# Kernel optimization log

Hardware: AMD Instinct MI355X
Metric: run time of the kernel (lower is better)

## Reference

```python
import jax, jax.numpy as jnp
import numpy as np

D, H, DK = 512, 8, 64
SCALE = 1.5 / 1.0  # gamma/tau, schedule='const'
NEG = -1e30


def _cross(x_q, x_kv, mask_kv, Wq, Wk, Wv, scale):
    # x_q: [B,Tq,D], x_kv: [B,Tk,D], mask_kv: [B,Tk] (1=keep, 0=mask)
    B, Tq, _ = x_q.shape
    Tk = x_kv.shape[1]
    q = (x_q @ Wq.T).reshape(B, Tq, H, DK).transpose(0, 2, 1, 3)
    k = (x_kv @ Wk.T).reshape(B, Tk, H, DK).transpose(0, 2, 1, 3)
    v = (x_kv @ Wv.T).reshape(B, Tk, H, DK).transpose(0, 2, 1, 3)
    logits = jnp.einsum('bhqd,bhkd->bhqk', q, k) * (scale / jnp.sqrt(jnp.float32(DK)))
    if mask_kv is not None:
        logits = jnp.where(mask_kv[:, None, None, :] == 0, NEG, logits)
    attn = jax.nn.softmax(logits, axis=-1)
    out = jnp.einsum('bhqk,bhkd->bhqd', attn, v)
    return out.transpose(0, 2, 1, 3).reshape(B, Tq, D)


def setup_inputs() -> dict:
    key = jax.random.key(0)
    ks = jax.random.split(key, 12)
    B, T = 4, 2048
    inp = {
        'skel_seq': jax.random.normal(ks[0], (B, T, D), jnp.float32),
        'sens_seq': jax.random.normal(ks[1], (B, T, D), jnp.float32),
        'mask_skel': jax.random.randint(ks[2], (B, T), 0, 2, jnp.int32),
        'mask_sens': jax.random.randint(ks[3], (B, T), 0, 2, jnp.int32),
    }
    s = 1.0 / np.sqrt(D)
    names = ['Wq_s2e', 'Wk_e', 'Wv_e', 'Wq_e2s', 'Wk_s', 'Wv_s', 'Wo_s', 'Wo_e']
    for i, n in enumerate(names):
        inp[n] = jax.random.normal(ks[4 + i], (D, D), jnp.float32) * s
    return inp


def reference(skel_seq, sens_seq, mask_skel, mask_sens,
              Wq_s2e, Wk_e, Wv_e, Wq_e2s, Wk_s, Wv_s, Wo_s, Wo_e):
    # skel queries attend over sensor keys/values
    s2e = _cross(skel_seq, sens_seq, mask_sens, Wq_s2e, Wk_e, Wv_e, SCALE) @ Wo_e.T
    # sensor queries attend over skeleton keys/values
    e2s = _cross(sens_seq, skel_seq, mask_skel, Wq_e2s, Wk_s, Wv_s, SCALE) @ Wo_s.T
    return (e2s, s2e)
```

## Files before the change

kernel.cpp:

```cpp
#include <hip/hip_runtime.h>
#include <hip/hip_bf16.h>

#define T_SEQ 2048
#define N_TOK 4194304
#define W_ELEM 262144


typedef float f32x4  __attribute__((ext_vector_type(4)));
typedef short bf16x8 __attribute__((ext_vector_type(8)));

#define SCALE_Q 0.27050532f

__device__ __forceinline__ unsigned short f2b(float f) {
    __hip_bfloat16 h = __float2bfloat16(f);
    return *reinterpret_cast<unsigned short*>(&h);
}

__device__ __forceinline__ int pack2bf(float lo, float hi) {
    return ((int)f2b(hi) << 16) | (int)f2b(lo);
}

__device__ __forceinline__ bf16x8 ldg8(const unsigned short* p) {
    union { int4 i; bf16x8 b; } u;
    u.i = *reinterpret_cast<const int4*>(p);
    return u.b;
}

__device__ __forceinline__ float fexp2(float x) {
#if __has_builtin(__builtin_amdgcn_exp2f)
    return __builtin_amdgcn_exp2f(x);
#else
    return exp2f(x);
#endif
}

typedef unsigned int u32_g __attribute__((address_space(1)));
typedef unsigned int u32_l __attribute__((address_space(3)));
__device__ __forceinline__ void gload_lds16(const void* g, void* l) {
    __builtin_amdgcn_global_load_lds((const u32_g*)g, (u32_l*)l, 16, 0, 0);
}

__global__ __launch_bounds__(256)
void prep_bias(const int* __restrict__ ms, const int* __restrict__ mk,
               float* __restrict__ dst)
{
    const int i = (blockIdx.x * 256 + threadIdx.x) * 8;
    const int* m = (i >> 13) ? mk : ms;
    const int rem = i & 8191;
    const int4 a = *reinterpret_cast<const int4*>(&m[rem]);
    const int4 b = *reinterpret_cast<const int4*>(&m[rem + 4]);
    float4 f0, f1;
    f0.x = a.x ? 0.0f : -3e38f; f0.y = a.y ? 0.0f : -3e38f;
    f0.z = a.z ? 0.0f : -3e38f; f0.w = a.w ? 0.0f : -3e38f;
    f1.x = b.x ? 0.0f : -3e38f; f1.y = b.y ? 0.0f : -3e38f;
    f1.z = b.z ? 0.0f : -3e38f; f1.w = b.w ? 0.0f : -3e38f;
    *reinterpret_cast<float4*>(&dst[i])     = f0;
    *reinterpret_cast<float4*>(&dst[i + 4]) = f1;
}

__global__ __launch_bounds__(256)
void to_bf16(const float* __restrict__ s0, const float* __restrict__ s1,
             const float* __restrict__ w0, const float* __restrict__ w1,
             const float* __restrict__ w2, const float* __restrict__ w3,
             const float* __restrict__ w4, const float* __restrict__ w5,
             unsigned short* __restrict__ dst)
{
    const int y = blockIdx.y;
    const float* src;
    size_t off; int n;
    switch (y) {
        case 0: src = s0; off = 0;                          n = N_TOK;  break;
        case 1: src = s1; off = N_TOK;                      n = N_TOK;  break;
        case 2: src = w0; off = 2 * (size_t)N_TOK;              n = W_ELEM; break;
        case 3: src = w1; off = 2 * (size_t)N_TOK + 1 * W_ELEM; n = W_ELEM; break;
        case 4: src = w2; off = 2 * (size_t)N_TOK + 2 * W_ELEM; n = W_ELEM; break;
        case 5: src = w3; off = 2 * (size_t)N_TOK + 3 * W_ELEM; n = W_ELEM; break;
        case 6: src = w4; off = 2 * (size_t)N_TOK + 4 * W_ELEM; n = W_ELEM; break;
        default: src = w5; off = 2 * (size_t)N_TOK + 5 * W_ELEM; n = W_ELEM; break;
    }
    const int idx = (blockIdx.x * 256 + threadIdx.x) * 8;
    if (idx >= n) return;
    const float4 a = *reinterpret_cast<const float4*>(src + idx);
    const float4 b = *reinterpret_cast<const float4*>(src + idx + 4);
    int4 o;
    o.x = pack2bf(a.x, a.y); o.y = pack2bf(a.z, a.w);
    o.z = pack2bf(b.x, b.y); o.w = pack2bf(b.z, b.w);
    *reinterpret_cast<int4*>(dst + off + idx) = o;
}

#define MF_SETUP                                                               \
    __shared__ short Asm[64][72];                                              \
    __shared__ short Wsm[64][72];                                              \
    const int tid  = threadIdx.x;                                              \
    const int lane = tid & 63;                                                 \
    const int w4   = tid >> 6;                                                 \
    const int nl   = lane & 15;                                                \
    const int quad = lane >> 4;                                                \
    const int n0 = blockIdx.x * 64;                                            \
    const int m0 = blockIdx.y * 64;                                            \
    const int arow = tid >> 2;                                                 \
    const int acol = (tid & 3) * 16;                                           \
    f32x4 acc[4] = {};

#define MF_WRITE_W                                                             \
    {                                                                          \
        int4 x;                                                                \
        x.x = pack2bf(wv[0].x, wv[0].y); x.y = pack2bf(wv[0].z, wv[0].w);      \
        x.z = pack2bf(wv[1].x, wv[1].y); x.w = pack2bf(wv[1].z, wv[1].w);      \
        *reinterpret_cast<int4*>(&Wsm[arow][acol]) = x;                        \
        x.x = pack2bf(wv[2].x, wv[2].y); x.y = pack2bf(wv[2].z, wv[2].w);      \
        x.z = pack2bf(wv[3].x, wv[3].y); x.w = pack2bf(wv[3].z, wv[3].w);      \
        *reinterpret_cast<int4*>(&Wsm[arow][acol + 8]) = x;                    \
    }

#define MF_MMA_LOOP                                                            \
    _Pragma("unroll")                                                          \
    for (int kc = 0; kc < 2; ++kc) {                                           \
        const bf16x8 a = *reinterpret_cast<const bf16x8*>(                     \
            &Asm[w4 * 16 + nl][kc * 32 + quad * 8]);                           \
        _Pragma("unroll")                                                      \
        for (int c = 0; c < 4; ++c) {                                          \
            const bf16x8 bf = *reinterpret_cast<const bf16x8*>(                \
                &Wsm[c * 16 + nl][kc * 32 + quad * 8]);                        \
            acc[c] = __builtin_amdgcn_mfma_f32_16x16x32_bf16(a, bf, acc[c],    \
                                                             0, 0, 0);         \
        }                                                                      \
    }

#define MF_CWRITE_PROJ                                                         \
    if (!trans) {                                                              \
        _Pragma("unroll")                                                      \
        for (int c = 0; c < 4; ++c)                                            \
            _Pragma("unroll")                                                  \
            for (int r = 0; r < 4; ++r)                                        \
                C[(size_t)(m0 + w4 * 16 + quad * 4 + r) * 512 + n0 + c * 16 + nl] = \
                    f2b(acc[c][r] * alpha);                                    \
    } else {                                                                   \
        const int b  = m0 >> 11;                                               \
        const int t0 = (m0 & 2047) + w4 * 16 + quad * 4;                       \
        _Pragma("unroll")                                                      \
        for (int c = 0; c < 4; ++c) {                                          \
            const int n = n0 + c * 16 + nl;                                    \
            ushort4 o;                                                         \
            o.x = f2b(acc[c][0]);                                              \
            o.y = f2b(acc[c][1]);                                              \
            o.z = f2b(acc[c][2]);                                              \
            o.w = f2b(acc[c][3]);                                              \
            *reinterpret_cast<ushort4*>(C + (size_t)(b * 512 + n) * T_SEQ + t0) = o; \
        }                                                                      \
    }

__global__ __launch_bounds__(256)
void proj_all(const float* __restrict__ skel, const float* __restrict__ sens,
              const float* __restrict__ Wq1, const float* __restrict__ Wk1,
              const float* __restrict__ Wv1, const float* __restrict__ Wq2,
              const float* __restrict__ Wk2, const float* __restrict__ Wv2,
              unsigned short* __restrict__ Q1, unsigned short* __restrict__ K1,
              unsigned short* __restrict__ Vt1, unsigned short* __restrict__ Q2,
              unsigned short* __restrict__ K2, unsigned short* __restrict__ Vt2,
              int zbase)
{
    const int z = zbase + blockIdx.z;
    const float* A; const float* W; unsigned short* C;
    float alpha = 1.0f; bool trans = false;
    switch (z) {
        case 0:  A = skel; W = Wq1; C = Q1; alpha = SCALE_Q; break;
        case 1:  A = sens; W = Wk1; C = K1; break;
        case 2:  A = sens; W = Wv1; C = Vt1; trans = true; break;
        case 3:  A = sens; W = Wq2; C = Q2; alpha = SCALE_Q; break;
        case 4:  A = skel; W = Wk2; C = K2; break;
        default: A = skel; W = Wv2; C = Vt2; trans = true; break;
    }

    MF_SETUP
    const float* ap = A + (size_t)(m0 + arow) * 512 + acol;
    const float* wp = W + (size_t)(n0 + arow) * 512 + acol;
    float4 av[4], wv[4];
    #pragma unroll
    for (int j = 0; j < 4; ++j) {
        av[j] = *reinterpret_cast<const float4*>(ap + 4 * j);
        wv[j] = *reinterpret_cast<const float4*>(wp + 4 * j);
    }
    for (int it = 0; it < 8; ++it) {
        __syncthreads();
        {
            int4 x;
            x.x = pack2bf(av[0].x, av[0].y); x.y = pack2bf(av[0].z, av[0].w);
            x.z = pack2bf(av[1].x, av[1].y); x.w = pack2bf(av[1].z, av[1].w);
            *reinterpret_cast<int4*>(&Asm[arow][acol]) = x;
            x.x = pack2bf(av[2].x, av[2].y); x.y = pack2bf(av[2].z, av[2].w);
            x.z = pack2bf(av[3].x, av[3].y); x.w = pack2bf(av[3].z, av[3].w);
            *reinterpret_cast<int4*>(&Asm[arow][acol + 8]) = x;
        }
        MF_WRITE_W
        __syncthreads();
        if (it < 7) {
            const float* apn = ap + (it + 1) * 64;
            const float* wpn = wp + (it + 1) * 64;
            #pragma unroll
            for (int j = 0; j < 4; ++j) {
                av[j] = *reinterpret_cast<const float4*>(apn + 4 * j);
                wv[j] = *reinterpret_cast<const float4*>(wpn + 4 * j);
            }
        }
        MF_MMA_LOOP
    }
    MF_CWRITE_PROJ
}

__global__ __launch_bounds__(256, 2)
void proj_fused(const unsigned short* __restrict__ skb,
                const unsigned short* __restrict__ snb,
                const unsigned short* __restrict__ wball,
                unsigned short* __restrict__ Q1, unsigned short* __restrict__ K1,
                unsigned short* __restrict__ Vt1, unsigned short* __restrict__ Q2,
                unsigned short* __restrict__ K2, unsigned short* __restrict__ Vt2)
{
    __shared__ short Al[2][64][64];
    __shared__ short Wl[2][256][64];

    const int o  = blockIdx.x;
    const int wg = (o & 7) * 192 + (o >> 3);
    const int z  = wg >> 8;
    const int mt = (wg >> 1) & 127;
    const int xh = wg & 1;

    const unsigned short* A = (z == 0 || z >= 4) ? skb : snb;
    const unsigned short* W = wball + (size_t)z * W_ELEM;
    unsigned short* C;
    switch (z) {
        case 0: C = Q1;  break;
        case 1: C = K1;  break;
        case 2: C = Vt1; break;
        case 3: C = Q2;  break;
        case 4: C = K2;  break;
        default: C = Vt2; break;
    }
    const bool trans = (z == 2 || z == 5);
    const float alpha = (z == 0 || z == 3) ? SCALE_Q : 1.0f;

    const int tid  = threadIdx.x;
    const int w    = tid >> 6;
    const int lane = tid & 63;
    const int nl   = lane & 15;
    const int quad = lane >> 4;
    const int r8   = lane >> 3;
    const int cg   = (lane & 7) ^ r8;

    const int m0g = mt * 64;
    const int n0  = xh * 256;

    const unsigned short* Ab = A + (size_t)m0g * 512 + cg * 8;
    const unsigned short* Wb = W + (size_t)n0  * 512 + cg * 8;

    f32x4 acc[16] = {};

    auto stage = [&](int it, int buf) {
        const int k0 = it * 64;
        #pragma unroll
        for (int g = 0; g < 2; ++g) {
            const int rr = w * 16 + g * 8;
            gload_lds16(Ab + (size_t)(rr + r8) * 512 + k0, &Al[buf][rr][0]);
        }
        #pragma unroll
        for (int g = 0; g < 8; ++g) {
            const int rr = w * 64 + g * 8;
            gload_lds16(Wb + (size_t)(rr + r8) * 512 + k0, &Wl[buf][rr][0]);
        }
    };

    stage(0, 0);
    asm volatile("s_waitcnt vmcnt(0)" ::: "memory");
    __syncthreads();

    const int sw = nl & 7;
    for (int it = 0; it < 8; ++it) {
        const int buf = it & 1;
        if (it < 7) stage(it + 1, buf ^ 1);
        #pragma unroll
        for (int kc = 0; kc < 2; ++kc) {
            const bf16x8 a = *reinterpret_cast<const bf16x8*>(
                &Al[buf][w * 16 + nl][((kc * 4 + quad) ^ sw) * 8]);
            #pragma unroll
            for (int c = 0; c < 16; ++c) {
                const bf16x8 b = *reinterpret_cast<const bf16x8*>(
                    &Wl[buf][c * 16 + nl][((kc * 4 + quad) ^ sw) * 8]);
                acc[c] = __builtin_amdgcn_mfma_f32_16x16x32_bf16(a, b, acc[c],
                                                                 0, 0, 0);
            }
        }
        asm volatile("s_waitcnt vmcnt(0)" ::: "memory");
        __syncthreads();
    }

    short* ep = &Wl[0][0][0];
    if (!trans) {
        short (*Cl)[264] = reinterpret_cast<short (*)[264]>(ep);
        #pragma unroll
        for (int c = 0; c < 16; ++c)
            #pragma unroll
            for (int r = 0; r < 4; ++r)
                Cl[w * 16 + quad * 4 + r][c * 16 + nl] =
                    (short)f2b(acc[c][r] * alpha);
        __syncthreads();
        const int lr = tid >> 2;
        const int sb = (tid & 3) * 64;
        unsigned short* cp = C + (size_t)(m0g + lr) * 512 + n0 + sb;
        #pragma unroll
        for (int j = 0; j < 8; ++j)
            *reinterpret_cast<int4*>(cp + j * 8) =
                *reinterpret_cast<const int4*>(&Cl[lr][sb + j * 8]);
    } else {
        short (*Tl)[72] = reinterpret_cast<short (*)[72]>(ep);
        #pragma unroll
        for (int c = 0; c < 16; ++c) {
            int* dst = reinterpret_cast<int*>(&Tl[c * 16 + nl][w * 16 + quad * 4]);
            dst[0] = pack2bf(acc[c][0], acc[c][1]);
            dst[1] = pack2bf(acc[c][2], acc[c][3]);
        }
        __syncthreads();
        const int bq = m0g >> 11;
        const int t0 = m0g & 2047;
        #pragma unroll
        for (int g = 0; g < 4; ++g) {
            const int nr = g * 64 + (tid >> 2);
            const int tc = (tid & 3) * 16;
            unsigned short* vp = C + (size_t)(bq * 512 + n0 + nr) * T_SEQ + t0 + tc;
            *reinterpret_cast<int4*>(vp)     = *reinterpret_cast<const int4*>(&Tl[nr][tc]);
            *reinterpret_cast<int4*>(vp + 8) = *reinterpret_cast<const int4*>(&Tl[nr][tc + 8]);
        }
    }
}

__global__ __launch_bounds__(256, 2)
void out_fused(const unsigned short* __restrict__ AO1, const float* __restrict__ Wo1,
               float* __restrict__ C1,
               const unsigned short* __restrict__ AO2, const float* __restrict__ Wo2,
               float* __restrict__ C2)
{
    __shared__ __align__(16) char smem[81920];
    short (*Al)[64][64]  = reinterpret_cast<short (*)[64][64]>(smem);
    short (*Wl)[256][64] = reinterpret_cast<short (*)[256][64]>(smem + 16384);

    const int o  = blockIdx.x;
    const int wg = (o & 7) * 64 + (o >> 3);
    const int z  = wg >> 8;
    const int mt = (wg >> 1) & 127;
    const int xh = wg & 1;

    const unsigned short* A = z ? AO2 : AO1;
    const float* W = z ? Wo2 : Wo1;
    float* C = z ? C2 : C1;

    const int tid  = threadIdx.x;
    const int w    = tid >> 6;
    const int lane = tid & 63;
    const int nl   = lane & 15;
    const int quad = lane >> 4;
    const int r8   = lane >> 3;
    const int cg   = (lane & 7) ^ r8;

    const int m0g = mt * 64;
    const int n0  = xh * 256;

    const unsigned short* Ab = A + (size_t)m0g * 512 + cg * 8;

    const int rw_ = tid >> 2;
    const int cw_ = (tid & 3) * 4;

    f32x4 acc[16] = {};
    float4 wreg[4][4];

    auto stageA = [&](int it, int buf) {
        const int k0 = it * 64;
        #pragma unroll
        for (int g = 0; g < 2; ++g) {
            const int rr = w * 16 + g * 8;
            gload_lds16(Ab + (size_t)(rr + r8) * 512 + k0, &Al[buf][rr][0]);
        }
    };
    auto wload = [&](int it) {
        const int k0 = it * 64;
        #pragma unroll
        for (int g = 0; g < 4; ++g) {
            const float* wp = W + (size_t)(n0 + g * 64 + rw_) * 512 + k0 + cw_;
            #pragma unroll
            for (int j = 0; j < 4; ++j)
                wreg[g][j] = *reinterpret_cast<const float4*>(wp + 16 * j);
        }
    };
    auto wstore = [&](int buf) {
        const int key = rw_ & 7;
        #pragma unroll
        for (int g = 0; g < 4; ++g) {
            const int r = g * 64 + rw_;
            #pragma unroll
            for (int j = 0; j < 4; ++j) {
                int2 pk;
                pk.x = pack2bf(wreg[g][j].x, wreg[g][j].y);
                pk.y = pack2bf(wreg[g][j].z, wreg[g][j].w);
                const int slot = (2 * j + (cw_ >> 3)) ^ key;
                *reinterpret_cast<int2*>(
                    &Wl[buf][r][slot * 8 + ((tid & 1) * 4)]) = pk;
            }
        }
    };

    wload(0);
    stageA(0, 0);
    asm volatile("s_waitcnt vmcnt(0)" ::: "memory");
    wstore(0);
    __syncthreads();

    const int sw = nl & 7;
    for (int it = 0; it < 8; ++it) {
        const int buf = it & 1;
        if (it < 7) { stageA(it + 1, buf ^ 1); wload(it + 1); }
        #pragma unroll
        for (int kc = 0; kc < 2; ++kc) {
            const bf16x8 a = *reinterpret_cast<const bf16x8*>(
                &Al[buf][w * 16 + nl][((kc * 4 + quad) ^ sw) * 8]);
            #pragma unroll
            for (int c = 0; c < 16; ++c) {
                const bf16x8 b = *reinterpret_cast<const bf16x8*>(
                    &Wl[buf][c * 16 + nl][((kc * 4 + quad) ^ sw) * 8]);
                acc[c] = __builtin_amdgcn_mfma_f32_16x16x32_bf16(a, b, acc[c],
                                                                 0, 0, 0);
            }
        }
        asm volatile("s_waitcnt vmcnt(0)" ::: "memory");
        if (it < 7) wstore(buf ^ 1);
        __syncthreads();
    }

    float (*Cl)[264] = reinterpret_cast<float (*)[264]>(smem);
    #pragma unroll
    for (int c = 0; c < 16; ++c)
        #pragma unroll
        for (int r = 0; r < 4; ++r)
            Cl[w * 16 + quad * 4 + r][c * 16 + nl] = acc[c][r];
    __syncthreads();
    const int rr2 = tid >> 3;
    const int lc  = (tid & 7) * 4;
    #pragma unroll
    for (int pass = 0; pass < 2; ++pass) {
        const int row = pass * 32 + rr2;
        float* cp = C + (size_t)(m0g + row) * 512 + n0;
        #pragma unroll
        for (int j = 0; j < 8; ++j)
            *reinterpret_cast<float4*>(cp + lc + j * 32) =
                *reinterpret_cast<const float4*>(&Cl[row][lc + j * 32]);
    }
}

__global__ __launch_bounds__(256)
void out_proj(const unsigned short* __restrict__ AO1, const float* __restrict__ Wo1,
              float* __restrict__ C1,
              const unsigned short* __restrict__ AO2, const float* __restrict__ Wo2,
              float* __restrict__ C2, int zbase)
{
    const int z = zbase + blockIdx.z;
    const unsigned short* A = z ? AO2 : AO1;
    const float* W = z ? Wo2 : Wo1;
    float* C = z ? C2 : C1;

    MF_SETUP
    const unsigned short* ap = A + (size_t)(m0 + arow) * 512 + acol;
    const float* wp = W + (size_t)(n0 + arow) * 512 + acol;
    int4 ai[2];
    float4 wv[4];
    ai[0] = *reinterpret_cast<const int4*>(ap);
    ai[1] = *reinterpret_cast<const int4*>(ap + 8);
    #pragma unroll
    for (int j = 0; j < 4; ++j)
        wv[j] = *reinterpret_cast<const float4*>(wp + 4 * j);
    for (int it = 0; it < 8; ++it) {
        __syncthreads();
        *reinterpret_cast<int4*>(&Asm[arow][acol])     = ai[0];
        *reinterpret_cast<int4*>(&Asm[arow][acol + 8]) = ai[1];
        MF_WRITE_W
        __syncthreads();
        if (it < 7) {
            const unsigned short* apn = ap + (it + 1) * 64;
            const float* wpn = wp + (it + 1) * 64;
            ai[0] = *reinterpret_cast<const int4*>(apn);
            ai[1] = *reinterpret_cast<const int4*>(apn + 8);
            #pragma unroll
            for (int j = 0; j < 4; ++j)
                wv[j] = *reinterpret_cast<const float4*>(wpn + 4 * j);
        }
        MF_MMA_LOOP
    }
    #pragma unroll
    for (int c = 0; c < 4; ++c)
        #pragma unroll
        for (int r = 0; r < 4; ++r)
            C[(size_t)(m0 + w4 * 16 + quad * 4 + r) * 512 + n0 + c * 16 + nl] =
                acc[c][r];
}

__global__ __launch_bounds__(512)
void attn_mfma(const unsigned short* Q1x, const unsigned short* __restrict__ K1x,
               const unsigned short* __restrict__ V1x, const float* __restrict__ b1x,
               unsigned short* AO1x,
               const unsigned short* Q2x, const unsigned short* __restrict__ K2x,
               const unsigned short* __restrict__ V2x, const float* __restrict__ b2x,
               unsigned short* AO2x)
{
    __shared__ short Kl[2][64][64];
    __shared__ short Vl[2][64][64];
    __shared__ short Pl[8][16][64];

    const int dir = blockIdx.y >> 5;
    const unsigned short* Q  = dir ? Q2x : Q1x;
    const unsigned short* K  = dir ? K2x : K1x;
    const unsigned short* Vt = dir ? V2x : V1x;
    const float* biasD       = dir ? b2x : b1x;
    unsigned short* AO       = dir ? AO2x : AO1x;

    const int tid  = threadIdx.x;
    const int w    = tid >> 6;
    const int lane = tid & 63;
    const int nl   = lane & 15;
    const int quad = lane >> 4;
    const int qt = blockIdx.x;
    const int bh = blockIdx.y & 31;
    const int b = bh >> 3, h = bh & 7;
    const size_t tb = (size_t)b * (T_SEQ * 512);
    const float* biasB = biasD + b * T_SEQ;

    const int r8 = lane >> 3;
    const int cg = (lane & 7) ^ r8;
    const int sr = w * 8;

    const unsigned short* qp = Q + tb + (size_t)(qt * 128 + w * 16 + nl) * 512 + h * 64 + quad * 8;
    const bf16x8 qb0 = ldg8(qp);
    const bf16x8 qb1 = ldg8(qp + 32);

    float l_run = 0.0f;
    f32x4 o[4] = {};

    gload_lds16(K  + tb + (size_t)(sr + r8) * 512 + h * 64 + cg * 8, &Kl[0][sr][0]);
    gload_lds16(Vt + (size_t)(b * 512 + h * 64 + sr + r8) * T_SEQ + cg * 8, &Vl[0][sr][0]);
    asm volatile("s_waitcnt vmcnt(0)" ::: "memory");
    __syncthreads();

    const int swz = nl & 7;

    for (int kt = 0; kt < 32; ++kt) {
        const int cur = kt & 1;
        short (*Kb)[64] = Kl[cur];
        short (*Vb)[64] = Vl[cur];

        if (kt < 31) {
            short (*Kn)[64] = Kl[cur ^ 1];
            short (*Vn)[64] = Vl[cur ^ 1];
            gload_lds16(K  + tb + (size_t)((kt + 1) * 64 + sr + r8) * 512 + h * 64 + cg * 8, &Kn[sr][0]);
            gload_lds16(Vt + (size_t)(b * 512 + h * 64 + sr + r8) * T_SEQ + (size_t)(kt + 1) * 64 + cg * 8, &Vn[sr][0]);
        }

        float p[4][4];
        #pragma unroll
        for (int s = 0; s < 4; ++s) {
            const bf16x8 k0 = *reinterpret_cast<const bf16x8*>(&Kb[s * 16 + nl][(quad ^ swz) * 8]);
            const bf16x8 k1 = *reinterpret_cast<const bf16x8*>(&Kb[s * 16 + nl][((4 + quad) ^ swz) * 8]);
            const float4 bb = *reinterpret_cast<const float4*>(
                &biasB[kt * 64 + s * 16 + quad * 4]);
            f32x4 z = {bb.x, bb.y, bb.z, bb.w};
            z = __builtin_amdgcn_mfma_f32_16x16x32_bf16(k0, qb0, z, 0, 0, 0);
            z = __builtin_amdgcn_mfma_f32_16x16x32_bf16(k1, qb1, z, 0, 0, 0);
            p[s][0] = fexp2(z[0]);
            p[s][1] = fexp2(z[1]);
            p[s][2] = fexp2(z[2]);
            p[s][3] = fexp2(z[3]);
            l_run += p[s][0] + p[s][1] + p[s][2] + p[s][3];
        }

        #pragma unroll
        for (int s = 0; s < 4; ++s) {
            int2 pk;
            pk.x = pack2bf(p[s][0], p[s][1]);
            pk.y = pack2bf(p[s][2], p[s][3]);
            const int slot = (2 * s + (quad >> 1)) ^ swz;
            *reinterpret_cast<int2*>(&Pl[w][nl][slot * 8 + (quad & 1) * 4]) = pk;
        }

        const bf16x8 pa0 = *reinterpret_cast<const bf16x8*>(&Pl[w][nl][(quad ^ swz) * 8]);
        const bf16x8 pa1 = *reinterpret_cast<const bf16x8*>(&Pl[w][nl][((4 + quad) ^ swz) * 8]);
        __builtin_amdgcn_s_setprio(1);
        #pragma unroll
        for (int sd = 0; sd < 4; ++sd) {
            const bf16x8 v0 = *reinterpret_cast<const bf16x8*>(&Vb[sd * 16 + nl][(quad ^ swz) * 8]);
            const bf16x8 v1 = *reinterpret_cast<const bf16x8*>(&Vb[sd * 16 + nl][((4 + quad) ^ swz) * 8]);
            o[sd] = __builtin_amdgcn_mfma_f32_16x16x32_bf16(v0, pa0, o[sd], 0, 0, 0);
            o[sd] = __builtin_amdgcn_mfma_f32_16x16x32_bf16(v1, pa1, o[sd], 0, 0, 0);
        }
        __builtin_amdgcn_s_setprio(0);

        asm volatile("s_waitcnt vmcnt(0)" ::: "memory");
        __syncthreads();
    }

    l_run += __shfl_xor(l_run, 16);
    l_run += __shfl_xor(l_run, 32);
    const float inv = 1.0f / l_run;
    unsigned short* ob = AO + tb + (size_t)(qt * 128 + w * 16 + nl) * 512 + h * 64 + quad * 4;
    #pragma unroll
    for (int sd = 0; sd < 4; ++sd) {
        ushort4 o4;
        o4.x = f2b(o[sd][0] * inv);
        o4.y = f2b(o[sd][1] * inv);
        o4.z = f2b(o[sd][2] * inv);
        o4.w = f2b(o[sd][3] * inv);
        *reinterpret_cast<ushort4*>(ob + sd * 16) = o4;
    }
}

extern "C" void kernel_launch(void* const* d_in, const int* in_sizes, int n_in,
                              void* d_out, int out_size, void* d_ws, size_t ws_size,
                              hipStream_t stream) {
    const float* skel = (const float*)d_in[0];
    const float* sens = (const float*)d_in[1];
    const int* mask_skel = (const int*)d_in[2];
    const int* mask_sens = (const int*)d_in[3];
    const float* Wq_s2e = (const float*)d_in[4];
    const float* Wk_e   = (const float*)d_in[5];
    const float* Wv_e   = (const float*)d_in[6];
    const float* Wq_e2s = (const float*)d_in[7];
    const float* Wk_s   = (const float*)d_in[8];
    const float* Wv_s   = (const float*)d_in[9];
    const float* Wo_s   = (const float*)d_in[10];
    const float* Wo_e   = (const float*)d_in[11];
    float* out = (float*)d_out;

    unsigned short* Q1 = (unsigned short*)d_ws;
    unsigned short* K1 = Q1 + N_TOK;
    unsigned short* V1 = K1 + N_TOK;

    const bool big = ws_size >= (size_t)6 * N_TOK * sizeof(unsigned short);

    if (big) {
        unsigned short* Q2 = V1 + N_TOK;
        unsigned short* K2 = Q2 + N_TOK;
        unsigned short* V2 = K2 + N_TOK;
        unsigned short* SC  = (unsigned short*)d_out;
        unsigned short* skb = SC;
        unsigned short* snb = SC + N_TOK;
        unsigned short* wb  = SC + 2 * (size_t)N_TOK;
        float* biasS = (float*)(SC + 2 * (size_t)N_TOK + 6 * W_ELEM);
        float* bias0 = biasS;
        float* bias1 = biasS + 4 * T_SEQ;
        prep_bias<<<dim3(8), 256, 0, stream>>>(mask_sens, mask_skel, biasS);
        to_bf16<<<dim3(2048, 8), 256, 0, stream>>>(
            skel, sens, Wq_s2e, Wk_e, Wv_e, Wq_e2s, Wk_s, Wv_s, SC);
        proj_fused<<<dim3(1536), 256, 0, stream>>>(
            skb, snb, wb, Q1, K1, V1, Q2, K2, V2);
        attn_mfma<<<dim3(16, 64), 512, 0, stream>>>(
            Q1, K1, V1, bias0, Q1,
            Q2, K2, V2, bias1, Q2);
        out_fused<<<dim3(512), 256, 0, stream>>>(
            Q1, Wo_e, out + N_TOK, Q2, Wo_s, out);
    } else {
        float* bias0 = out;
        float* bias1 = out + 8192;
        prep_bias<<<dim3(8), 256, 0, stream>>>(mask_sens, mask_skel, bias0);
        proj_all<<<dim3(8, 128, 3), 256, 0, stream>>>(
            skel, sens, Wq_s2e, Wk_e, Wv_e, Wq_e2s, Wk_s, Wv_s,
            Q1, K1, V1, Q1, K1, V1, 0);
        attn_mfma<<<dim3(16, 32), 512, 0, stream>>>(
            Q1, K1, V1, bias0, Q1, Q1, K1, V1, bias0, Q1);
        out_proj<<<dim3(8, 128, 1), 256, 0, stream>>>(
            Q1, Wo_e, out + N_TOK, Q1, Wo_s, out, 0);
        proj_all<<<dim3(8, 128, 3), 256, 0, stream>>>(
            skel, sens, Wq_s2e, Wk_e, Wv_e, Wq_e2s, Wk_s, Wv_s,
            Q1, K1, V1, Q1, K1, V1, 3);
        attn_mfma<<<dim3(16, 32), 512, 0, stream>>>(
            Q1, K1, V1, bias1, Q1, Q1, K1, V1, bias1, Q1);
        out_proj<<<dim3(8, 128, 1), 256, 0, stream>>>(
            Q1, Wo_s, out, Q1, Wo_s, out, 1);
    }
}
```

Before: 305.7 us.

## Retile projection GEMMs to 128x128 with 2x2 warp grid; compact to_bf16 grid

The fused QKV projection and output projection kernels move from 64x256 block tiles with one-row-strip-per-warp to 128x128 tiles with a 2x2 warp layout. Each warp now computes a 64x64 subtile, reusing 4 A and 4 B fragments across 16 MFMAs instead of 1 A against 16 B, which cuts LDS read traffic per MFMA. The epilogues and W fp32-to-bf16 staging are reworked to match. Separately, to_bf16 uses a flat 1D grid that launches only the needed blocks instead of an 8x2048 grid where most weight blocks exit early. LDS use per block changes, which may affect occupancy.

New measurement: 300.9 us. No clear change (-1.6%).

```diff
diff --git a/kernel.cpp b/kernel.cpp
--- a/kernel.cpp
+++ b/kernel.cpp
@@ -65,21 +65,23 @@
              const float* __restrict__ w4, const float* __restrict__ w5,
              unsigned short* __restrict__ dst)
 {
-    const int y = blockIdx.y;
+    const int bid = blockIdx.x;
+    int y, x;
+    if (bid < 4096) { y = bid >> 11; x = bid & 2047; }
+    else { const int t = bid - 4096; y = 2 + (t >> 7); x = t & 127; }
     const float* src;
-    size_t off; int n;
+    size_t off;
     switch (y) {
-        case 0: src = s0; off = 0;                          n = N_TOK;  break;
-        case 1: src = s1; off = N_TOK;                      n = N_TOK;  break;
-        case 2: src = w0; off = 2 * (size_t)N_TOK;              n = W_ELEM; break;
-        case 3: src = w1; off = 2 * (size_t)N_TOK + 1 * W_ELEM; n = W_ELEM; break;
-        case 4: src = w2; off = 2 * (size_t)N_TOK + 2 * W_ELEM; n = W_ELEM; break;
-        case 5: src = w3; off = 2 * (size_t)N_TOK + 3 * W_ELEM; n = W_ELEM; break;
-        case 6: src = w4; off = 2 * (size_t)N_TOK + 4 * W_ELEM; n = W_ELEM; break;
-        default: src = w5; off = 2 * (size_t)N_TOK + 5 * W_ELEM; n = W_ELEM; break;
-    }
-    const int idx = (blockIdx.x * 256 + threadIdx.x) * 8;
-    if (idx >= n) return;
+        case 0: src = s0; off = 0;      break;
+        case 1: src = s1; off = N_TOK;  break;
+        case 2: src = w0; off = 2 * (size_t)N_TOK;              break;
+        case 3: src = w1; off = 2 * (size_t)N_TOK + 1 * W_ELEM; break;
+        case 4: src = w2; off = 2 * (size_t)N_TOK + 2 * W_ELEM; break;
+        case 5: src = w3; off = 2 * (size_t)N_TOK + 3 * W_ELEM; break;
+        case 6: src = w4; off = 2 * (size_t)N_TOK + 4 * W_ELEM; break;
+        default: src = w5; off = 2 * (size_t)N_TOK + 5 * W_ELEM; break;
+    }
+    const int idx = (x * 256 + threadIdx.x) * 8;
     const float4 a = *reinterpret_cast<const float4*>(src + idx);
     const float4 b = *reinterpret_cast<const float4*>(src + idx + 4);
     int4 o;
@@ -216,14 +218,16 @@
                 unsigned short* __restrict__ Vt1, unsigned short* __restrict__ Q2,
                 unsigned short* __restrict__ K2, unsigned short* __restrict__ Vt2)
 {
-    __shared__ short Al[2][64][64];
-    __shared__ short Wl[2][256][64];
-
-    const int o  = blockIdx.x;
-    const int wg = (o & 7) * 192 + (o >> 3);
-    const int z  = wg >> 8;
-    const int mt = (wg >> 1) & 127;
-    const int xh = wg & 1;
+    __shared__ __align__(16) char smem[65536];
+    short (*Al)[128][64] = reinterpret_cast<short (*)[128][64]>(smem);
+    short (*Wl)[128][64] = reinterpret_cast<short (*)[128][64]>(smem + 32768);
+
+    const int o   = blockIdx.x;
+    const int wg  = (o & 7) * 192 + (o >> 3);
+    const int z   = wg >> 8;
+    const int idx = wg & 255;
+    const int nh  = idx & 3;
+    const int mt  = idx >> 2;
 
     const unsigned short* A = (z == 0 || z >= 4) ? skb : snb;
     const unsigned short* W = wball + (size_t)z * W_ELEM;
@@ -241,30 +245,28 @@
 
     const int tid  = threadIdx.x;
     const int w    = tid >> 6;
+    const int wr   = w >> 1;
+    const int wc   = w & 1;
     const int lane = tid & 63;
     const int nl   = lane & 15;
     const int quad = lane >> 4;
     const int r8   = lane >> 3;
     const int cg   = (lane & 7) ^ r8;
 
-    const int m0g = mt * 64;
-    const int n0  = xh * 256;
+    const int m0g = mt * 128;
+    const int n0  = nh * 128;
 
     const unsigned short* Ab = A + (size_t)m0g * 512 + cg * 8;
     const unsigned short* Wb = W + (size_t)n0  * 512 + cg * 8;
 
-    f32x4 acc[16] = {};
+    f32x4 acc[4][4] = {};
 
     auto stage = [&](int it, int buf) {
         const int k0 = it * 64;
         #pragma unroll
-        for (int g = 0; g < 2; ++g) {
-            const int rr = w * 16 + g * 8;
+        for (int g = 0; g < 4; ++g) {
+            const int rr = w * 32 + g * 8;
             gload_lds16(Ab + (size_t)(rr + r8) * 512 + k0, &Al[buf][rr][0]);
-        }
-        #pragma unroll
-        for (int g = 0; g < 8; ++g) {
-            const int rr = w * 64 + g * 8;
             gload_lds16(Wb + (size_t)(rr + r8) * 512 + k0, &Wl[buf][rr][0]);
         }
     };
@@ -279,56 +281,65 @@
         if (it < 7) stage(it + 1, buf ^ 1);
         #pragma unroll
         for (int kc = 0; kc < 2; ++kc) {
-            const bf16x8 a = *reinterpret_cast<const bf16x8*>(
-                &Al[buf][w * 16 + nl][((kc * 4 + quad) ^ sw) * 8]);
-            #pragma unroll
-            for (int c = 0; c < 16; ++c) {
-                const bf16x8 b = *reinterpret_cast<const bf16x8*>(
-                    &Wl[buf][c * 16 + nl][((kc * 4 + quad) ^ sw) * 8]);
-                acc[c] = __builtin_amdgcn_mfma_f32_16x16x32_bf16(a, b, acc[c],
-                                                                 0, 0, 0);
-            }
+            bf16x8 a[4], bb[4];
+            #pragma unroll
+            for (int am = 0; am < 4; ++am)
+                a[am] = *reinterpret_cast<const bf16x8*>(
+                    &Al[buf][wr * 64 + am * 16 + nl][((kc * 4 + quad) ^ sw) * 8]);
+            #pragma unroll
+            for (int bn = 0; bn < 4; ++bn)
+                bb[bn] = *reinterpret_cast<const bf16x8*>(
+                    &Wl[buf][wc * 64 + bn * 16 + nl][((kc * 4 + quad) ^ sw) * 8]);
+            #pragma unroll
+            for (int am = 0; am < 4; ++am)
+                #pragma unroll
+                for (int bn = 0; bn < 4; ++bn)
+                    acc[am][bn] = __builtin_amdgcn_mfma_f32_16x16x32_bf16(
+                        a[am], bb[bn], acc[am][bn], 0, 0, 0);
         }
         asm volatile("s_waitcnt vmcnt(0)" ::: "memory");
         __syncthreads();
     }
 
-    short* ep = &Wl[0][0][0];
     if (!trans) {
-        short (*Cl)[264] = reinterpret_cast<short (*)[264]>(ep);
-        #pragma unroll
-        for (int c = 0; c < 16; ++c)
-            #pragma unroll
-            for (int r = 0; r < 4; ++r)
-                Cl[w * 16 + quad * 4 + r][c * 16 + nl] =
-                    (short)f2b(acc[c][r] * alpha);
-        __syncthreads();
-        const int lr = tid >> 2;
-        const int sb = (tid & 3) * 64;
-        unsigned short* cp = C + (size_t)(m0g + lr) * 512 + n0 + sb;
+        short (*Cl)[132] = reinterpret_cast<short (*)[132]>(smem);
+        #pragma unroll
+        for (int am = 0; am < 4; ++am)
+            #pragma unroll
+            for (int bn = 0; bn < 4; ++bn)
+                #pragma unroll
+                for (int r = 0; r < 4; ++r)
+                    Cl[wr * 64 + am * 16 + quad * 4 + r][wc * 64 + bn * 16 + nl] =
+                        (short)f2b(acc[am][bn][r] * alpha);
+        __syncthreads();
+        const int lr = tid >> 1;
+        const int ch = (tid & 1) * 64;
+        unsigned short* cp = C + (size_t)(m0g + lr) * 512 + n0 + ch;
         #pragma unroll
         for (int j = 0; j < 8; ++j)
             *reinterpret_cast<int4*>(cp + j * 8) =
-                *reinterpret_cast<const int4*>(&Cl[lr][sb + j * 8]);
+                *reinterpret_cast<const int4*>(&Cl[lr][ch + j * 8]);
     } else {
-        short (*Tl)[72] = reinterpret_cast<short (*)[72]>(ep);
-        #pragma unroll
-        for (int c = 0; c < 16; ++c) {
-            int* dst = reinterpret_cast<int*>(&Tl[c * 16 + nl][w * 16 + quad * 4]);
-            dst[0] = pack2bf(acc[c][0], acc[c][1]);
-            dst[1] = pack2bf(acc[c][2], acc[c][3]);
-        }
+        short (*Tl)[132] = reinterpret_cast<short (*)[132]>(smem);
+        #pragma unroll
+        for (int am = 0; am < 4; ++am)
+            #pragma unroll
+            for (int bn = 0; bn < 4; ++bn) {
+                int* dst = reinterpret_cast<int*>(
+                    &Tl[wc * 64 + bn * 16 + nl][wr * 64 + am * 16 + quad * 4]);
+                dst[0] = pack2bf(acc[am][bn][0], acc[am][bn][1]);
+                dst[1] = pack2bf(acc[am][bn][2], acc[am][bn][3]);
+            }
         __syncthreads();
         const int bq = m0g >> 11;
         const int t0 = m0g & 2047;
-        #pragma unroll
-        for (int g = 0; g < 4; ++g) {
-            const int nr = g * 64 + (tid >> 2);
-            const int tc = (tid & 3) * 16;
-            unsigned short* vp = C + (size_t)(bq * 512 + n0 + nr) * T_SEQ + t0 + tc;
-            *reinterpret_cast<int4*>(vp)     = *reinterpret_cast<const int4*>(&Tl[nr][tc]);
-            *reinterpret_cast<int4*>(vp + 8) = *reinterpret_cast<const int4*>(&Tl[nr][tc + 8]);
-        }
+        const int nr = tid >> 1;
+        const int tc = (tid & 1) * 64;
+        unsigned short* vp = C + (size_t)(bq * 512 + n0 + nr) * T_SEQ + t0 + tc;
+        #pragma unroll
+        for (int j = 0; j < 8; ++j)
+            *reinterpret_cast<int4*>(vp + j * 8) =
+                *reinterpret_cast<const int4*>(&Tl[nr][tc + j * 8]);
     }
 }
 
@@ -338,15 +349,16 @@
                const unsigned short* __restrict__ AO2, const float* __restrict__ Wo2,
                float* __restrict__ C2)
 {
-    __shared__ __align__(16) char smem[81920];
-    short (*Al)[64][64]  = reinterpret_cast<short (*)[64][64]>(smem);
-    short (*Wl)[256][64] = reinterpret_cast<short (*)[256][64]>(smem + 16384);
-
-    const int o  = blockIdx.x;
-    const int wg = (o & 7) * 64 + (o >> 3);
-    const int z  = wg >> 8;
-    const int mt = (wg >> 1) & 127;
-    const int xh = wg & 1;
+    __shared__ __align__(16) char smem[67584];
+    short (*Al)[128][64] = reinterpret_cast<short (*)[128][64]>(smem);
+    short (*Wl)[128][64] = reinterpret_cast<short (*)[128][64]>(smem + 32768);
+
+    const int o   = blockIdx.x;
+    const int wg  = (o & 7) * 64 + (o >> 3);
+    const int z   = wg >> 8;
+    const int idx = wg & 255;
+    const int nh  = idx & 3;
+    const int mt  = idx >> 2;
 
     const unsigned short* A = z ? AO2 : AO1;
     const float* W = z ? Wo2 : Wo1;
@@ -354,55 +366,49 @@
 
     const int tid  = threadIdx.x;
     const int w    = tid >> 6;
+    const int wr   = w >> 1;
+    const int wc   = w & 1;
     const int lane = tid & 63;
     const int nl   = lane & 15;
     const int quad = lane >> 4;
     const int r8   = lane >> 3;
     const int cg   = (lane & 7) ^ r8;
 
-    const int m0g = mt * 64;
-    const int n0  = xh * 256;
+    const int m0g = mt * 128;
+    const int n0  = nh * 128;
 
     const unsigned short* Ab = A + (size_t)m0g * 512 + cg * 8;
 
-    const int rw_ = tid >> 2;
-    const int cw_ = (tid & 3) * 4;
-
-    f32x4 acc[16] = {};
-    float4 wreg[4][4];
+    const int rw_ = tid >> 1;
+    const int ch_ = (tid & 1) * 32;
+    const int key = rw_ & 7;
+
+    f32x4 acc[4][4] = {};
+    float4 wreg[8];
 
     auto stageA = [&](int it, int buf) {
         const int k0 = it * 64;
         #pragma unroll
-        for (int g = 0; g < 2; ++g) {
-            const int rr = w * 16 + g * 8;
+        for (int g = 0; g < 4; ++g) {
+            const int rr = w * 32 + g * 8;
             gload_lds16(Ab + (size_t)(rr + r8) * 512 + k0, &Al[buf][rr][0]);
         }
     };
     auto wload = [&](int it) {
-        const int k0 = it * 64;
-        #pragma unroll
-        for (int g = 0; g < 4; ++g) {
-            const float* wp = W + (size_t)(n0 + g * 64 + rw_) * 512 + k0 + cw_;
-            #pragma unroll
-            for (int j = 0; j < 4; ++j)
-                wreg[g][j] = *reinterpret_cast<const float4*>(wp + 16 * j);
-        }
+        const float* wp = W + (size_t)(n0 + rw_) * 512 + it * 64 + ch_;
+        #pragma unroll
+        for (int j = 0; j < 8; ++j)
+            wreg[j] = *reinterpret_cast<const float4*>(wp + 4 * j);
     };
     auto wstore = [&](int buf) {
-        const int key = rw_ & 7;
-        #pragma unroll
-        for (int g = 0; g < 4; ++g) {
-            const int r = g * 64 + rw_;
-            #pragma unroll
-            for (int j = 0; j < 4; ++j) {
-                int2 pk;
-                pk.x = pack2bf(wreg[g][j].x, wreg[g][j].y);
-                pk.y = pack2bf(wreg[g][j].z, wreg[g][j].w);
-                const int slot = (2 * j + (cw_ >> 3)) ^ key;
-                *reinterpret_cast<int2*>(
-                    &Wl[buf][r][slot * 8 + ((tid & 1) * 4)]) = pk;
-            }
+        #pragma unroll
+        for (int j = 0; j < 8; ++j) {
+            int2 pk;
+            pk.x = pack2bf(wreg[j].x, wreg[j].y);
+            pk.y = pack2bf(wreg[j].z, wreg[j].w);
+            const int slot = ((tid & 1) * 4 + (j >> 1)) ^ key;
+            *reinterpret_cast<int2*>(
+                &Wl[buf][rw_][slot * 8 + (j & 1) * 4]) = pk;
         }
     };
 
@@ -418,39 +424,44 @@
         if (it < 7) { stageA(it + 1, buf ^ 1); wload(it + 1); }
         #pragma unroll
         for (int kc = 0; kc < 2; ++kc) {
-            const bf16x8 a = *reinterpret_cast<const bf16x8*>(
-                &Al[buf][w * 16 + nl][((kc * 4 + quad) ^ sw) * 8]);
-            #pragma unroll
-            for (int c = 0; c < 16; ++c) {
-                const bf16x8 b = *reinterpret_cast<const bf16x8*>(
-                    &Wl[buf][c * 16 + nl][((kc * 4 + quad) ^ sw) * 8]);
-                acc[c] = __builtin_amdgcn_mfma_f32_16x16x32_bf16(a, b, acc[c],
-                                                                 0, 0, 0);
-            }
+            bf16x8 a[4], bb[4];
+            #pragma unroll
+            for (int am = 0; am < 4; ++am)
+                a[am] = *reinterpret_cast<const bf16x8*>(
+                    &Al[buf][wr * 64 + am * 16 + nl][((kc * 4 + quad) ^ sw) * 8]);
+            #pragma unroll
+            for (int bn = 0; bn < 4; ++bn)
+                bb[bn] = *reinterpret_cast<const bf16x8*>(
+                    &Wl[buf][wc * 64 + bn * 16 + nl][((kc * 4 + quad) ^ sw) * 8]);
+            #pragma unroll
+            for (int am = 0; am < 4; ++am)
+                #pragma unroll
+                for (int bn = 0; bn < 4; ++bn)
+                    acc[am][bn] = __builtin_amdgcn_mfma_f32_16x16x32_bf16(
+                        a[am], bb[bn], acc[am][bn], 0, 0, 0);
         }
         asm volatile("s_waitcnt vmcnt(0)" ::: "memory");
         if (it < 7) wstore(buf ^ 1);
         __syncthreads();
     }
 
-    float (*Cl)[264] = reinterpret_cast<float (*)[264]>(smem);
+    float (*Cl)[132] = reinterpret_cast<float (*)[132]>(smem);
     #pragma unroll
-    for (int c = 0; c < 16; ++c)
-        #pragma unroll
-        for (int r = 0; r < 4; ++r)
-            Cl[w * 16 + quad * 4 + r][c * 16 + nl] = acc[c][r];
+    for (int am = 0; am < 4; ++am)
+        #pragma unroll
+        for (int bn = 0; bn < 4; ++bn)
+            #pragma unroll
+            for (int r = 0; r < 4; ++r)
+                Cl[wr * 64 + am * 16 + quad * 4 + r][wc * 64 + bn * 16 + nl] =
+                    acc[am][bn][r];
     __syncthreads();
-    const int rr2 = tid >> 3;
-    const int lc  = (tid & 7) * 4;
+    const int lr = tid >> 1;
+    const int fc = (tid & 1) * 64;
+    float* cp = C + (size_t)(m0g + lr) * 512 + n0 + fc;
     #pragma unroll
-    for (int pass = 0; pass < 2; ++pass) {
-        const int row = pass * 32 + rr2;
-        float* cp = C + (size_t)(m0g + row) * 512 + n0;
-        #pragma unroll
-        for (int j = 0; j < 8; ++j)
-            *reinterpret_cast<float4*>(cp + lc + j * 32) =
-                *reinterpret_cast<const float4*>(&Cl[row][lc + j * 32]);
-    }
+    for (int j = 0; j < 16; ++j)
+        *reinterpret_cast<float4*>(cp + j * 4) =
+            *reinterpret_cast<const float4*>(&Cl[lr][fc + j * 4]);
 }
 
 __global__ __launch_bounds__(256)
@@ -651,7 +662,7 @@
         float* bias0 = biasS;
         float* bias1 = biasS + 4 * T_SEQ;
         prep_bias<<<dim3(8), 256, 0, stream>>>(mask_sens, mask_skel, biasS);
-        to_bf16<<<dim3(2048, 8), 256, 0, stream>>>(
+        to_bf16<<<dim3(4864), 256, 0, stream>>>(
             skel, sens, Wq_s2e, Wk_e, Wv_e, Wq_e2s, Wk_s, Wv_s, SC);
         proj_fused<<<dim3(1536), 256, 0, stream>>>(
             skb, snb, wb, Q1, K1, V1, Q2, K2, V2);
```
